# Kernel optimization log

Measured on AMD Instinct MI355X. Metric: run time of the kernel, lower is better.

## Reference

```python
import jax, jax.numpy as jnp
import numpy as np

N_NODES = 50000
N_EDGES = 800000
D_IN = 64
D_HID = 64
D_OUT = 64


def setup_inputs() -> dict:
    key = jax.random.key(0)
    ks = jax.random.split(key, 10)
    x = jax.random.normal(ks[0], (N_NODES, D_IN), dtype=jnp.float32)
    src = jax.random.randint(ks[1], (N_EDGES,), 0, N_NODES, dtype=jnp.int32)
    dst = jax.random.randint(ks[2], (N_EDGES,), 0, N_NODES, dtype=jnp.int32)
    s = 1.0 / np.sqrt(D_IN)
    W0 = jax.random.uniform(ks[3], (D_IN, D_HID), jnp.float32, -s, s)
    b0 = jnp.zeros((D_HID,), jnp.float32)
    W1 = jax.random.uniform(ks[4], (D_HID, D_HID), jnp.float32, -s, s)
    b1 = jnp.zeros((D_HID,), jnp.float32)
    W2 = jax.random.uniform(ks[5], (D_HID, D_OUT), jnp.float32, -s, s)
    b2 = jnp.zeros((D_OUT,), jnp.float32)
    return {"x": x, "src": src, "dst": dst, "W0": W0, "b0": b0,
            "W1": W1, "b1": b1, "W2": W2, "b2": b2}


def reference(x, src, dst, W0, b0, W1, b1, W2, b2):
    N = x.shape[0]
    # in-degree (constant across layers)
    deg = jax.ops.segment_sum(jnp.ones(src.shape[0], x.dtype), dst, num_segments=N)
    inv = (1.0 / (deg + 1.0))[:, None]  # [N,1] gcn normalizer (deg + self)

    def sage_gcn(h, W, b):
        # gather neighbor feats along edges, scatter-add to destinations
        agg = jax.ops.segment_sum(h[src], dst, num_segments=N)  # [N,d]
        h_neigh = (agg + h) * inv
        return h_neigh @ W + b

    h = sage_gcn(x, W0, b0)
    h = jax.nn.relu(h)
    h = sage_gcn(h, W1, b1)
    h = jax.nn.relu(h)
    h = sage_gcn(h, W2, b2)
    return h
```

## Files before the change

kernel.cpp:

```cpp
#include <hip/hip_runtime.h>

#define D 64

__global__ void count_deg_kernel(const int* __restrict__ dst, int* __restrict__ deg, int nE) {
    int e4 = (blockIdx.x * blockDim.x + threadIdx.x) * 4;
    if (e4 + 3 < nE) {
        int4 d = *(const int4*)(dst + e4);
        atomicAdd(&deg[d.x], 1);
        atomicAdd(&deg[d.y], 1);
        atomicAdd(&deg[d.z], 1);
        atomicAdd(&deg[d.w], 1);
    } else {
        for (int e = e4; e < nE; ++e) atomicAdd(&deg[dst[e]], 1);
    }
}

__global__ __launch_bounds__(256) void scan_a_kernel(const int* __restrict__ deg,
                                                     int* __restrict__ row_ptr,
                                                     int* __restrict__ blocksums, int N) {
    __shared__ int s[256];
    int t = threadIdx.x;
    int i = blockIdx.x * 256 + t;
    int v = (i < N) ? deg[i] : 0;
    s[t] = v;
    __syncthreads();
    #pragma unroll
    for (int d = 1; d < 256; d <<= 1) {
        int u = (t >= d) ? s[t - d] : 0;
        __syncthreads();
        s[t] += u;
        __syncthreads();
    }
    if (i < N) row_ptr[i] = s[t] - v;
    if (t == 255) blocksums[blockIdx.x] = s[255];
}

__global__ __launch_bounds__(256) void scan_b_kernel(int* __restrict__ blocksums,
                                                     int* __restrict__ row_ptr,
                                                     int nb, int N) {
    __shared__ int s[256];
    int t = threadIdx.x;
    int v = (t < nb) ? blocksums[t] : 0;
    s[t] = v;
    __syncthreads();
    #pragma unroll
    for (int d = 1; d < 256; d <<= 1) {
        int u = (t >= d) ? s[t - d] : 0;
        __syncthreads();
        s[t] += u;
        __syncthreads();
    }
    if (t < nb) blocksums[t] = s[t] - v;
    if (t == 255) row_ptr[N] = s[255];
}

__global__ __launch_bounds__(256) void scan_c_kernel(int* __restrict__ row_ptr,
                                                     int* __restrict__ cursor,
                                                     const int* __restrict__ blocksums, int N) {
    int i = blockIdx.x * 256 + threadIdx.x;
    if (i < N) {
        int r = row_ptr[i] + blocksums[blockIdx.x];
        row_ptr[i] = r;
        cursor[i] = r;
    }
}

__global__ __launch_bounds__(256) void fill_csr_sliced_kernel(
    const int* __restrict__ src, const int* __restrict__ dst,
    int* __restrict__ cursor, int* __restrict__ col,
    int nE, int slice_size)
{
    const int g  = blockIdx.x & 7;
    const int gb = blockIdx.x >> 3;
    const int lo = g * slice_size;
    const int hi = lo + slice_size;
    int e4 = (gb * 256 + (int)threadIdx.x) * 4;
    if (e4 + 3 < nE) {
        int4 d = *(const int4*)(dst + e4);
        bool m0 = (d.x >= lo) & (d.x < hi);
        bool m1 = (d.y >= lo) & (d.y < hi);
        bool m2 = (d.z >= lo) & (d.z < hi);
        bool m3 = (d.w >= lo) & (d.w < hi);
        if (m0 | m1 | m2 | m3) {
            int4 s = *(const int4*)(src + e4);
            if (m0) col[atomicAdd(&cursor[d.x], 1)] = s.x;
            if (m1) col[atomicAdd(&cursor[d.y], 1)] = s.y;
            if (m2) col[atomicAdd(&cursor[d.z], 1)] = s.z;
            if (m3) col[atomicAdd(&cursor[d.w], 1)] = s.w;
        }
    } else if (e4 < nE) {
        for (int e = e4; e < nE; ++e) {
            int dd = dst[e];
            if (dd >= lo && dd < hi) col[atomicAdd(&cursor[dd], 1)] = src[e];
        }
    }
}

__global__ __launch_bounds__(256, 4) void sage_layer_kernel(
    const float* __restrict__ h, const int* __restrict__ row_ptr,
    const int* __restrict__ col, const float* __restrict__ W,
    const float* __restrict__ bias, float* __restrict__ out,
    int N, int do_relu)
{
    const int lane = threadIdx.x & 63;
    const int sub  = lane >> 4;
    const int fq   = lane & 15;
    const int w    = threadIdx.x >> 6;

    float Wreg[D];
    #pragma unroll
    for (int k = 0; k < D; ++k) Wreg[k] = W[k * D + lane];
    const float bj = bias[lane];

    const float4* __restrict__ h4 = (const float4*)h;

    const int nwaves = gridDim.x * 4;
    for (int i0 = blockIdx.x * 4 + w; i0 < N; i0 += nwaves) {
        const int i   = __builtin_amdgcn_readfirstlane(i0);
        const int rs  = __builtin_amdgcn_readfirstlane(row_ptr[i]);
        const int re  = __builtin_amdgcn_readfirstlane(row_ptr[i + 1]);
        const int deg = re - rs;

        float4 a0 = {0,0,0,0}, a1 = {0,0,0,0}, a2 = {0,0,0,0}, a3 = {0,0,0,0};

        for (int e0 = rs; e0 < re; e0 += 64) {
            int ee = e0 + lane;
            int idxv = col[(ee < re) ? ee : (re - 1)];
            int rem = re - e0;
            int steps = (((rem < 64) ? rem : 64) + 3) >> 2;
            int t = 0;
            for (; t + 4 <= steps; t += 4) {
                int base = (t << 2) + sub;
                int s0 = __shfl(idxv, base);
                int s1 = __shfl(idxv, base + 4);
                int s2 = __shfl(idxv, base + 8);
                int s3 = __shfl(idxv, base + 12);
                float4 v0 = h4[(size_t)s0 * 16 + fq];
                float4 v1 = h4[(size_t)s1 * 16 + fq];
                float4 v2 = h4[(size_t)s2 * 16 + fq];
                float4 v3 = h4[(size_t)s3 * 16 + fq];
                a0.x += v0.x; a0.y += v0.y; a0.z += v0.z; a0.w += v0.w;
                a1.x += v1.x; a1.y += v1.y; a1.z += v1.z; a1.w += v1.w;
                a2.x += v2.x; a2.y += v2.y; a2.z += v2.z; a2.w += v2.w;
                a3.x += v3.x; a3.y += v3.y; a3.z += v3.z; a3.w += v3.w;
            }
            for (; t < steps; ++t) {
                int s0 = __shfl(idxv, (t << 2) + sub);
                float4 v0 = h4[(size_t)s0 * 16 + fq];
                a0.x += v0.x; a0.y += v0.y; a0.z += v0.z; a0.w += v0.w;
            }
        }

        float4 tt;
        tt.x = (a0.x + a1.x) + (a2.x + a3.x);
        tt.y = (a0.y + a1.y) + (a2.y + a3.y);
        tt.z = (a0.z + a1.z) + (a2.z + a3.z);
        tt.w = (a0.w + a1.w) + (a2.w + a3.w);
        tt.x += __shfl_xor(tt.x, 16); tt.x += __shfl_xor(tt.x, 32);
        tt.y += __shfl_xor(tt.y, 16); tt.y += __shfl_xor(tt.y, 32);
        tt.z += __shfl_xor(tt.z, 16); tt.z += __shfl_xor(tt.z, 32);
        tt.w += __shfl_xor(tt.w, 16); tt.w += __shfl_xor(tt.w, 32);

        int pad = (-deg) & 3;
        if (deg > 0 && pad) {
            int last = __builtin_amdgcn_readfirstlane(col[re - 1]);
            float4 vl = h4[(size_t)last * 16 + fq];
            float fp = (float)pad;
            tt.x = fmaf(-fp, vl.x, tt.x);
            tt.y = fmaf(-fp, vl.y, tt.y);
            tt.z = fmaf(-fp, vl.z, tt.z);
            tt.w = fmaf(-fp, vl.w, tt.w);
        }

        float4 hs = h4[(size_t)i * 16 + fq];
        float invd = 1.0f / (float)(deg + 1);
        tt.x = (tt.x + hs.x) * invd;
        tt.y = (tt.y + hs.y) * invd;
        tt.z = (tt.z + hs.z) * invd;
        tt.w = (tt.w + hs.w) * invd;

        float o = bj;
        #pragma unroll
        for (int k = 0; k < D; ++k) {
            float comp = ((k & 3) == 0) ? tt.x : ((k & 3) == 1) ? tt.y
                       : ((k & 3) == 2) ? tt.z : tt.w;
            int ti = __builtin_amdgcn_readlane(__float_as_int(comp), k >> 2);
            o = fmaf(__int_as_float(ti), Wreg[k], o);
        }
        if (do_relu) o = fmaxf(o, 0.0f);
        out[(size_t)i * D + lane] = o;
    }
}

extern "C" void kernel_launch(void* const* d_in, const int* in_sizes, int n_in,
                              void* d_out, int out_size, void* d_ws, size_t ws_size,
                              hipStream_t stream) {
    const float* x   = (const float*)d_in[0];
    const int*   src = (const int*)d_in[1];
    const int*   dst = (const int*)d_in[2];
    const float* W0  = (const float*)d_in[3];
    const float* b0  = (const float*)d_in[4];
    const float* W1  = (const float*)d_in[5];
    const float* b1  = (const float*)d_in[6];
    const float* W2  = (const float*)d_in[7];
    const float* b2  = (const float*)d_in[8];
    float* out = (float*)d_out;

    const int N = in_sizes[0] / D;
    const int E = in_sizes[1];

    const int scan_blocks = (N + 255) / 256;

    char* ws = (char*)d_ws;
    size_t off = 0;
    auto alloc = [&](size_t bytes) -> void* {
        void* p = ws + off;
        off = (off + bytes + 255) & ~(size_t)255;
        return p;
    };
    int*   deg       = (int*)  alloc((size_t)N * sizeof(int));
    int*   row_ptr   = (int*)  alloc((size_t)(N + 1) * sizeof(int));
    int*   cursor    = (int*)  alloc((size_t)N * sizeof(int));
    int*   blocksums = (int*)  alloc((size_t)scan_blocks * sizeof(int));
    int*   col       = (int*)  alloc((size_t)E * sizeof(int));
    float* h1        = (float*)alloc((size_t)N * D * sizeof(float));
    float* h2        = (float*)alloc((size_t)N * D * sizeof(float));

    hipMemsetAsync(deg, 0, (size_t)N * sizeof(int), stream);
    const int e4_blocks = (E / 4 + 255) / 256;
    count_deg_kernel<<<e4_blocks, 256, 0, stream>>>(dst, deg, E);
    scan_a_kernel<<<scan_blocks, 256, 0, stream>>>(deg, row_ptr, blocksums, N);
    scan_b_kernel<<<1, 256, 0, stream>>>(blocksums, row_ptr, scan_blocks, N);
    scan_c_kernel<<<scan_blocks, 256, 0, stream>>>(row_ptr, cursor, blocksums, N);
    const int slice_size = (N + 7) / 8;
    fill_csr_sliced_kernel<<<e4_blocks * 8, 256, 0, stream>>>(src, dst, cursor, col, E, slice_size);

    const int layer_blocks = 4096;

    sage_layer_kernel<<<layer_blocks, 256, 0, stream>>>(x,  row_ptr, col, W0, b0, h1,  N, 1);
    sage_layer_kernel<<<layer_blocks, 256, 0, stream>>>(h1, row_ptr, col, W1, b1, h2,  N, 1);
    sage_layer_kernel<<<layer_blocks, 256, 0, stream>>>(h2, row_ptr, col, W2, b2, out, N, 0);
}
```

Measured before the change: 289.0 us.

## Process two nodes per wave and slice degree counting by destination range

```diff
diff --git a/kernel.cpp b/kernel.cpp
--- a/kernel.cpp
+++ b/kernel.cpp
@@ -2,16 +2,24 @@
 
 #define D 64
 
-__global__ void count_deg_kernel(const int* __restrict__ dst, int* __restrict__ deg, int nE) {
-    int e4 = (blockIdx.x * blockDim.x + threadIdx.x) * 4;
+__global__ void count_deg_sliced_kernel(const int* __restrict__ dst, int* __restrict__ deg,
+                                        int nE, int slice_size) {
+    const int g  = blockIdx.x & 7;
+    const int gb = blockIdx.x >> 3;
+    const int lo = g * slice_size;
+    const int hi = lo + slice_size;
+    int e4 = (gb * 256 + (int)threadIdx.x) * 4;
     if (e4 + 3 < nE) {
         int4 d = *(const int4*)(dst + e4);
-        atomicAdd(&deg[d.x], 1);
-        atomicAdd(&deg[d.y], 1);
-        atomicAdd(&deg[d.z], 1);
-        atomicAdd(&deg[d.w], 1);
-    } else {
-        for (int e = e4; e < nE; ++e) atomicAdd(&deg[dst[e]], 1);
+        if (d.x >= lo && d.x < hi) atomicAdd(&deg[d.x], 1);
+        if (d.y >= lo && d.y < hi) atomicAdd(&deg[d.y], 1);
+        if (d.z >= lo && d.z < hi) atomicAdd(&deg[d.z], 1);
+        if (d.w >= lo && d.w < hi) atomicAdd(&deg[d.w], 1);
+    } else if (e4 < nE) {
+        for (int e = e4; e < nE; ++e) {
+            int dd = dst[e];
+            if (dd >= lo && dd < hi) atomicAdd(&deg[dd], 1);
+        }
     }
 }
 
@@ -106,89 +114,147 @@
     const int sub  = lane >> 4;
     const int fq   = lane & 15;
     const int w    = threadIdx.x >> 6;
-
-    float Wreg[D];
-    #pragma unroll
-    for (int k = 0; k < D; ++k) Wreg[k] = W[k * D + lane];
     const float bj = bias[lane];
 
     const float4* __restrict__ h4 = (const float4*)h;
-
     const int nwaves = gridDim.x * 4;
-    for (int i0 = blockIdx.x * 4 + w; i0 < N; i0 += nwaves) {
-        const int i   = __builtin_amdgcn_readfirstlane(i0);
-        const int rs  = __builtin_amdgcn_readfirstlane(row_ptr[i]);
-        const int re  = __builtin_amdgcn_readfirstlane(row_ptr[i + 1]);
-        const int deg = re - rs;
-
-        float4 a0 = {0,0,0,0}, a1 = {0,0,0,0}, a2 = {0,0,0,0}, a3 = {0,0,0,0};
-
-        for (int e0 = rs; e0 < re; e0 += 64) {
-            int ee = e0 + lane;
-            int idxv = col[(ee < re) ? ee : (re - 1)];
-            int rem = re - e0;
-            int steps = (((rem < 64) ? rem : 64) + 3) >> 2;
-            int t = 0;
-            for (; t + 4 <= steps; t += 4) {
-                int base = (t << 2) + sub;
-                int s0 = __shfl(idxv, base);
-                int s1 = __shfl(idxv, base + 4);
-                int s2 = __shfl(idxv, base + 8);
-                int s3 = __shfl(idxv, base + 12);
-                float4 v0 = h4[(size_t)s0 * 16 + fq];
-                float4 v1 = h4[(size_t)s1 * 16 + fq];
-                float4 v2 = h4[(size_t)s2 * 16 + fq];
-                float4 v3 = h4[(size_t)s3 * 16 + fq];
-                a0.x += v0.x; a0.y += v0.y; a0.z += v0.z; a0.w += v0.w;
-                a1.x += v1.x; a1.y += v1.y; a1.z += v1.z; a1.w += v1.w;
-                a2.x += v2.x; a2.y += v2.y; a2.z += v2.z; a2.w += v2.w;
-                a3.x += v3.x; a3.y += v3.y; a3.z += v3.z; a3.w += v3.w;
+
+    for (int p = (blockIdx.x * 4 + w) * 2; p < N; p += nwaves * 2) {
+        const int iA = __builtin_amdgcn_readfirstlane(p);
+        const int iB = iA + 1;
+        const bool hasB = (iB < N);
+
+        const int rsA = __builtin_amdgcn_readfirstlane(row_ptr[iA]);
+        const int reA = __builtin_amdgcn_readfirstlane(row_ptr[iA + 1]);
+        const int reB = hasB ? __builtin_amdgcn_readfirstlane(row_ptr[iB + 1]) : reA;
+        const int rsB = reA;
+        const int degA = reA - rsA;
+        const int degB = reB - rsB;
+
+        float4 aA0 = {0,0,0,0}, aA1 = {0,0,0,0}, aA2 = {0,0,0,0}, aA3 = {0,0,0,0};
+        float4 aB0 = {0,0,0,0}, aB1 = {0,0,0,0}, aB2 = {0,0,0,0}, aB3 = {0,0,0,0};
+
+        int eA = rsA, eB = rsB;
+        while ((eA < reA) | (eB < reB)) {
+            int idxA = 0, idxB = 0;
+            if (eA < reA) { int ee = eA + lane; idxA = col[(ee < reA) ? ee : (reA - 1)]; }
+            if (eB < reB) { int ee = eB + lane; idxB = col[(ee < reB) ? ee : (reB - 1)]; }
+
+            if (eA < reA) {
+                int rem = reA - eA;
+                int steps = (((rem < 64) ? rem : 64) + 3) >> 2;
+                int t = 0;
+                for (; t + 4 <= steps; t += 4) {
+                    int base = (t << 2) + sub;
+                    int s0 = __shfl(idxA, base);
+                    int s1 = __shfl(idxA, base + 4);
+                    int s2 = __shfl(idxA, base + 8);
+                    int s3 = __shfl(idxA, base + 12);
+                    float4 v0 = h4[(size_t)s0 * 16 + fq];
+                    float4 v1 = h4[(size_t)s1 * 16 + fq];
+                    float4 v2 = h4[(size_t)s2 * 16 + fq];
+                    float4 v3 = h4[(size_t)s3 * 16 + fq];
+                    aA0.x += v0.x; aA0.y += v0.y; aA0.z += v0.z; aA0.w += v0.w;
+                    aA1.x += v1.x; aA1.y += v1.y; aA1.z += v1.z; aA1.w += v1.w;
+                    aA2.x += v2.x; aA2.y += v2.y; aA2.z += v2.z; aA2.w += v2.w;
+                    aA3.x += v3.x; aA3.y += v3.y; aA3.z += v3.z; aA3.w += v3.w;
+                }
+                for (; t < steps; ++t) {
+                    int s0 = __shfl(idxA, (t << 2) + sub);
+                    float4 v0 = h4[(size_t)s0 * 16 + fq];
+                    aA0.x += v0.x; aA0.y += v0.y; aA0.z += v0.z; aA0.w += v0.w;
+                }
             }
-            for (; t < steps; ++t) {
-                int s0 = __shfl(idxv, (t << 2) + sub);
-                float4 v0 = h4[(size_t)s0 * 16 + fq];
-                a0.x += v0.x; a0.y += v0.y; a0.z += v0.z; a0.w += v0.w;
+            if (eB < reB) {
+                int rem = reB - eB;
+                int steps = (((rem < 64) ? rem : 64) + 3) >> 2;
+                int t = 0;
+                for (; t + 4 <= steps; t += 4) {
+                    int base = (t << 2) + sub;
+                    int s0 = __shfl(idxB, base);
+                    int s1 = __shfl(idxB, base + 4);
+                    int s2 = __shfl(idxB, base + 8);
+                    int s3 = __shfl(idxB, base + 12);
+                    float4 v0 = h4[(size_t)s0 * 16 + fq];
+                    float4 v1 = h4[(size_t)s1 * 16 + fq];
+                    float4 v2 = h4[(size_t)s2 * 16 + fq];
+                    float4 v3 = h4[(size_t)s3 * 16 + fq];
+                    aB0.x += v0.x; aB0.y += v0.y; aB0.z += v0.z; aB0.w += v0.w;
+                    aB1.x += v1.x; aB1.y += v1.y; aB1.z += v1.z; aB1.w += v1.w;
+                    aB2.x += v2.x; aB2.y += v2.y; aB2.z += v2.z; aB2.w += v2.w;
+                    aB3.x += v3.x; aB3.y += v3.y; aB3.z += v3.z; aB3.w += v3.w;
+                }
+                for (; t < steps; ++t) {
+                    int s0 = __shfl(idxB, (t << 2) + sub);
+                    float4 v0 = h4[(size_t)s0 * 16 + fq];
+                    aB0.x += v0.x; aB0.y += v0.y; aB0.z += v0.z; aB0.w += v0.w;
+                }
             }
-        }
-
-        float4 tt;
-        tt.x = (a0.x + a1.x) + (a2.x + a3.x);
-        tt.y = (a0.y + a1.y) + (a2.y + a3.y);
-        tt.z = (a0.z + a1.z) + (a2.z + a3.z);
-        tt.w = (a0.w + a1.w) + (a2.w + a3.w);
-        tt.x += __shfl_xor(tt.x, 16); tt.x += __shfl_xor(tt.x, 32);
-        tt.y += __shfl_xor(tt.y, 16); tt.y += __shfl_xor(tt.y, 32);
-        tt.z += __shfl_xor(tt.z, 16); tt.z += __shfl_xor(tt.z, 32);
-        tt.w += __shfl_xor(tt.w, 16); tt.w += __shfl_xor(tt.w, 32);
-
-        int pad = (-deg) & 3;
-        if (deg > 0 && pad) {
-            int last = __builtin_amdgcn_readfirstlane(col[re - 1]);
+            eA += 64; eB += 64;
+        }
+
+        float4 tA, tB;
+        tA.x = (aA0.x + aA1.x) + (aA2.x + aA3.x);
+        tA.y = (aA0.y + aA1.y) + (aA2.y + aA3.y);
+        tA.z = (aA0.z + aA1.z) + (aA2.z + aA3.z);
+        tA.w = (aA0.w + aA1.w) + (aA2.w + aA3.w);
+        tB.x = (aB0.x + aB1.x) + (aB2.x + aB3.x);
+        tB.y = (aB0.y + aB1.y) + (aB2.y + aB3.y);
+        tB.z = (aB0.z + aB1.z) + (aB2.z + aB3.z);
+        tB.w = (aB0.w + aB1.w) + (aB2.w + aB3.w);
+        tA.x += __shfl_xor(tA.x, 16); tA.x += __shfl_xor(tA.x, 32);
+        tA.y += __shfl_xor(tA.y, 16); tA.y += __shfl_xor(tA.y, 32);
+        tA.z += __shfl_xor(tA.z, 16); tA.z += __shfl_xor(tA.z, 32);
+        tA.w += __shfl_xor(tA.w, 16); tA.w += __shfl_xor(tA.w, 32);
+        tB.x += __shfl_xor(tB.x, 16); tB.x += __shfl_xor(tB.x, 32);
+        tB.y += __shfl_xor(tB.y, 16); tB.y += __shfl_xor(tB.y, 32);
+        tB.z += __shfl_xor(tB.z, 16); tB.z += __shfl_xor(tB.z, 32);
+        tB.w += __shfl_xor(tB.w, 16); tB.w += __shfl_xor(tB.w, 32);
+
+        int padA = (-degA) & 3;
+        if (degA > 0 && padA) {
+            int last = __builtin_amdgcn_readfirstlane(col[reA - 1]);
             float4 vl = h4[(size_t)last * 16 + fq];
-            float fp = (float)pad;
-            tt.x = fmaf(-fp, vl.x, tt.x);
-            tt.y = fmaf(-fp, vl.y, tt.y);
-            tt.z = fmaf(-fp, vl.z, tt.z);
-            tt.w = fmaf(-fp, vl.w, tt.w);
-        }
-
-        float4 hs = h4[(size_t)i * 16 + fq];
-        float invd = 1.0f / (float)(deg + 1);
-        tt.x = (tt.x + hs.x) * invd;
-        tt.y = (tt.y + hs.y) * invd;
-        tt.z = (tt.z + hs.z) * invd;
-        tt.w = (tt.w + hs.w) * invd;
-
-        float o = bj;
+            float fp = (float)padA;
+            tA.x = fmaf(-fp, vl.x, tA.x); tA.y = fmaf(-fp, vl.y, tA.y);
+            tA.z = fmaf(-fp, vl.z, tA.z); tA.w = fmaf(-fp, vl.w, tA.w);
+        }
+        int padB = (-degB) & 3;
+        if (hasB && degB > 0 && padB) {
+            int last = __builtin_amdgcn_readfirstlane(col[reB - 1]);
+            float4 vl = h4[(size_t)last * 16 + fq];
+            float fp = (float)padB;
+            tB.x = fmaf(-fp, vl.x, tB.x); tB.y = fmaf(-fp, vl.y, tB.y);
+            tB.z = fmaf(-fp, vl.z, tB.z); tB.w = fmaf(-fp, vl.w, tB.w);
+        }
+
+        float4 hsA = h4[(size_t)iA * 16 + fq];
+        float invA = 1.0f / (float)(degA + 1);
+        tA.x = (tA.x + hsA.x) * invA; tA.y = (tA.y + hsA.y) * invA;
+        tA.z = (tA.z + hsA.z) * invA; tA.w = (tA.w + hsA.w) * invA;
+        if (hasB) {
+            float4 hsB = h4[(size_t)iB * 16 + fq];
+            float invB = 1.0f / (float)(degB + 1);
+            tB.x = (tB.x + hsB.x) * invB; tB.y = (tB.y + hsB.y) * invB;
+            tB.z = (tB.z + hsB.z) * invB; tB.w = (tB.w + hsB.w) * invB;
+        }
+
+        float oA = bj, oB = bj;
         #pragma unroll
         for (int k = 0; k < D; ++k) {
-            float comp = ((k & 3) == 0) ? tt.x : ((k & 3) == 1) ? tt.y
-                       : ((k & 3) == 2) ? tt.z : tt.w;
-            int ti = __builtin_amdgcn_readlane(__float_as_int(comp), k >> 2);
-            o = fmaf(__int_as_float(ti), Wreg[k], o);
-        }
-        if (do_relu) o = fmaxf(o, 0.0f);
-        out[(size_t)i * D + lane] = o;
+            float wv = W[k * D + lane];
+            float cA = ((k & 3) == 0) ? tA.x : ((k & 3) == 1) ? tA.y
+                     : ((k & 3) == 2) ? tA.z : tA.w;
+            float cB = ((k & 3) == 0) ? tB.x : ((k & 3) == 1) ? tB.y
+                     : ((k & 3) == 2) ? tB.z : tB.w;
+            int ia = __builtin_amdgcn_readlane(__float_as_int(cA), k >> 2);
+            int ib = __builtin_amdgcn_readlane(__float_as_int(cB), k >> 2);
+            oA = fmaf(__int_as_float(ia), wv, oA);
+            oB = fmaf(__int_as_float(ib), wv, oB);
+        }
+        if (do_relu) { oA = fmaxf(oA, 0.0f); oB = fmaxf(oB, 0.0f); }
+        out[(size_t)iA * D + lane] = oA;
+        if (hasB) out[(size_t)iB * D + lane] = oB;
     }
 }
 
@@ -228,14 +294,14 @@
 
     hipMemsetAsync(deg, 0, (size_t)N * sizeof(int), stream);
     const int e4_blocks = (E / 4 + 255) / 256;
-    count_deg_kernel<<<e4_blocks, 256, 0, stream>>>(dst, deg, E);
+    const int slice_size = (N + 7) / 8;
+    count_deg_sliced_kernel<<<e4_blocks * 8, 256, 0, stream>>>(dst, deg, E, slice_size);
     scan_a_kernel<<<scan_blocks, 256, 0, stream>>>(deg, row_ptr, blocksums, N);
     scan_b_kernel<<<1, 256, 0, stream>>>(blocksums, row_ptr, scan_blocks, N);
     scan_c_kernel<<<scan_blocks, 256, 0, stream>>>(row_ptr, cursor, blocksums, N);
-    const int slice_size = (N + 7) / 8;
     fill_csr_sliced_kernel<<<e4_blocks * 8, 256, 0, stream>>>(src, dst, cursor, col, E, slice_size);
 
-    const int layer_blocks = 4096;
+    const int layer_blocks = (N / 2 + 3) / 4;
 
     sage_layer_kernel<<<layer_blocks, 256, 0, stream>>>(x,  row_ptr, col, W0, b0, h1,  N, 1);
     sage_layer_kernel<<<layer_blocks, 256, 0, stream>>>(h1, row_ptr, col, W1, b1, h2,  N, 1);
```

Result: slower. 309.6 us (+7.1%).

## Split SAGE layer into column-chunked gather and separate MLP kernels

Applied to the files above, without the earlier changes.

```diff
diff --git a/kernel.cpp b/kernel.cpp
--- a/kernel.cpp
+++ b/kernel.cpp
@@ -2,16 +2,24 @@
 
 #define D 64
 
-__global__ void count_deg_kernel(const int* __restrict__ dst, int* __restrict__ deg, int nE) {
-    int e4 = (blockIdx.x * blockDim.x + threadIdx.x) * 4;
+__global__ void count_deg_sliced_kernel(const int* __restrict__ dst, int* __restrict__ deg,
+                                        int nE, int slice_size) {
+    const int g  = blockIdx.x & 7;
+    const int gb = blockIdx.x >> 3;
+    const int lo = g * slice_size;
+    const int hi = lo + slice_size;
+    int e4 = (gb * 256 + (int)threadIdx.x) * 4;
     if (e4 + 3 < nE) {
         int4 d = *(const int4*)(dst + e4);
-        atomicAdd(&deg[d.x], 1);
-        atomicAdd(&deg[d.y], 1);
-        atomicAdd(&deg[d.z], 1);
-        atomicAdd(&deg[d.w], 1);
-    } else {
-        for (int e = e4; e < nE; ++e) atomicAdd(&deg[dst[e]], 1);
+        if (d.x >= lo && d.x < hi) atomicAdd(&deg[d.x], 1);
+        if (d.y >= lo && d.y < hi) atomicAdd(&deg[d.y], 1);
+        if (d.z >= lo && d.z < hi) atomicAdd(&deg[d.z], 1);
+        if (d.w >= lo && d.w < hi) atomicAdd(&deg[d.w], 1);
+    } else if (e4 < nE) {
+        for (int e = e4; e < nE; ++e) {
+            int dd = dst[e];
+            if (dd >= lo && dd < hi) atomicAdd(&deg[dd], 1);
+        }
     }
 }
 
@@ -96,96 +104,95 @@
     }
 }
 
-__global__ __launch_bounds__(256, 4) void sage_layer_kernel(
+__global__ __launch_bounds__(256, 4) void sage_gather_kernel(
     const float* __restrict__ h, const int* __restrict__ row_ptr,
-    const int* __restrict__ col, const float* __restrict__ W,
+    const int* __restrict__ col, float* __restrict__ t, int N)
+{
+    const int g     = blockIdx.x & 7;
+    const int chunk = g & 3;
+    const int half  = g >> 2;
+    const int gb    = blockIdx.x >> 3;
+    const int lane  = threadIdx.x & 63;
+    const int sub   = lane >> 4;
+    const int f     = lane & 15;
+    const int fcol  = chunk * 16 + f;
+    const int w     = threadIdx.x >> 6;
+
+    const int Nh = (N + 1) >> 1;
+    const int lo = half * Nh;
+    const int hi = (lo + Nh < N) ? (lo + Nh) : N;
+    const int waves_per_group = (gridDim.x >> 3) * 4;
+
+    for (int i0 = lo + gb * 4 + w; i0 < hi; i0 += waves_per_group) {
+        const int i  = __builtin_amdgcn_readfirstlane(i0);
+        const int rs = __builtin_amdgcn_readfirstlane(row_ptr[i]);
+        const int re = __builtin_amdgcn_readfirstlane(row_ptr[i + 1]);
+        const int deg = re - rs;
+
+        float a0 = 0.f, a1 = 0.f, a2 = 0.f, a3 = 0.f;
+        for (int e0 = rs; e0 < re; e0 += 64) {
+            int ee = e0 + lane;
+            int idx = col[(ee < re) ? ee : (re - 1)];
+            int rem = re - e0;
+            int steps = (((rem < 64) ? rem : 64) + 3) >> 2;
+            int tt = 0;
+            for (; tt + 4 <= steps; tt += 4) {
+                int base = (tt << 2) + sub;
+                int s0 = __shfl(idx, base);
+                int s1 = __shfl(idx, base + 4);
+                int s2 = __shfl(idx, base + 8);
+                int s3 = __shfl(idx, base + 12);
+                a0 += h[(size_t)s0 * D + fcol];
+                a1 += h[(size_t)s1 * D + fcol];
+                a2 += h[(size_t)s2 * D + fcol];
+                a3 += h[(size_t)s3 * D + fcol];
+            }
+            for (; tt < steps; ++tt) {
+                int s0 = __shfl(idx, (tt << 2) + sub);
+                a0 += h[(size_t)s0 * D + fcol];
+            }
+        }
+
+        float tv = (a0 + a1) + (a2 + a3);
+        tv += __shfl_xor(tv, 16);
+        tv += __shfl_xor(tv, 32);
+
+        int pad = (-deg) & 3;
+        if (deg > 0 && pad) {
+            int last = __builtin_amdgcn_readfirstlane(col[re - 1]);
+            tv = fmaf(-(float)pad, h[(size_t)last * D + fcol], tv);
+        }
+        tv = (tv + h[(size_t)i * D + fcol]) * (1.0f / (float)(deg + 1));
+
+        if (lane < 16) t[(size_t)i * D + fcol] = tv;
+    }
+}
+
+__global__ __launch_bounds__(256) void sage_mlp_kernel(
+    const float* __restrict__ t, const float* __restrict__ W,
     const float* __restrict__ bias, float* __restrict__ out,
     int N, int do_relu)
 {
+    __shared__ float Ws[D * D];
+    for (int i = threadIdx.x; i < D * D; i += 256) Ws[i] = W[i];
     const int lane = threadIdx.x & 63;
-    const int sub  = lane >> 4;
     const int fq   = lane & 15;
     const int w    = threadIdx.x >> 6;
-
-    float Wreg[D];
-    #pragma unroll
-    for (int k = 0; k < D; ++k) Wreg[k] = W[k * D + lane];
     const float bj = bias[lane];
-
-    const float4* __restrict__ h4 = (const float4*)h;
-
+    __syncthreads();
+
+    const float4* __restrict__ t4 = (const float4*)t;
     const int nwaves = gridDim.x * 4;
     for (int i0 = blockIdx.x * 4 + w; i0 < N; i0 += nwaves) {
-        const int i   = __builtin_amdgcn_readfirstlane(i0);
-        const int rs  = __builtin_amdgcn_readfirstlane(row_ptr[i]);
-        const int re  = __builtin_amdgcn_readfirstlane(row_ptr[i + 1]);
-        const int deg = re - rs;
-
-        float4 a0 = {0,0,0,0}, a1 = {0,0,0,0}, a2 = {0,0,0,0}, a3 = {0,0,0,0};
-
-        for (int e0 = rs; e0 < re; e0 += 64) {
-            int ee = e0 + lane;
-            int idxv = col[(ee < re) ? ee : (re - 1)];
-            int rem = re - e0;
-            int steps = (((rem < 64) ? rem : 64) + 3) >> 2;
-            int t = 0;
-            for (; t + 4 <= steps; t += 4) {
-                int base = (t << 2) + sub;
-                int s0 = __shfl(idxv, base);
-                int s1 = __shfl(idxv, base + 4);
-                int s2 = __shfl(idxv, base + 8);
-                int s3 = __shfl(idxv, base + 12);
-                float4 v0 = h4[(size_t)s0 * 16 + fq];
-                float4 v1 = h4[(size_t)s1 * 16 + fq];
-                float4 v2 = h4[(size_t)s2 * 16 + fq];
-                float4 v3 = h4[(size_t)s3 * 16 + fq];
-                a0.x += v0.x; a0.y += v0.y; a0.z += v0.z; a0.w += v0.w;
-                a1.x += v1.x; a1.y += v1.y; a1.z += v1.z; a1.w += v1.w;
-                a2.x += v2.x; a2.y += v2.y; a2.z += v2.z; a2.w += v2.w;
-                a3.x += v3.x; a3.y += v3.y; a3.z += v3.z; a3.w += v3.w;
-            }
-            for (; t < steps; ++t) {
-                int s0 = __shfl(idxv, (t << 2) + sub);
-                float4 v0 = h4[(size_t)s0 * 16 + fq];
-                a0.x += v0.x; a0.y += v0.y; a0.z += v0.z; a0.w += v0.w;
-            }
-        }
-
-        float4 tt;
-        tt.x = (a0.x + a1.x) + (a2.x + a3.x);
-        tt.y = (a0.y + a1.y) + (a2.y + a3.y);
-        tt.z = (a0.z + a1.z) + (a2.z + a3.z);
-        tt.w = (a0.w + a1.w) + (a2.w + a3.w);
-        tt.x += __shfl_xor(tt.x, 16); tt.x += __shfl_xor(tt.x, 32);
-        tt.y += __shfl_xor(tt.y, 16); tt.y += __shfl_xor(tt.y, 32);
-        tt.z += __shfl_xor(tt.z, 16); tt.z += __shfl_xor(tt.z, 32);
-        tt.w += __shfl_xor(tt.w, 16); tt.w += __shfl_xor(tt.w, 32);
-
-        int pad = (-deg) & 3;
-        if (deg > 0 && pad) {
-            int last = __builtin_amdgcn_readfirstlane(col[re - 1]);
-            float4 vl = h4[(size_t)last * 16 + fq];
-            float fp = (float)pad;
-            tt.x = fmaf(-fp, vl.x, tt.x);
-            tt.y = fmaf(-fp, vl.y, tt.y);
-            tt.z = fmaf(-fp, vl.z, tt.z);
-            tt.w = fmaf(-fp, vl.w, tt.w);
-        }
-
-        float4 hs = h4[(size_t)i * 16 + fq];
-        float invd = 1.0f / (float)(deg + 1);
-        tt.x = (tt.x + hs.x) * invd;
-        tt.y = (tt.y + hs.y) * invd;
-        tt.z = (tt.z + hs.z) * invd;
-        tt.w = (tt.w + hs.w) * invd;
-
+        const int i = __builtin_amdgcn_readfirstlane(i0);
+        float4 tv = t4[(size_t)i * 16 + fq];
         float o = bj;
         #pragma unroll
         for (int k = 0; k < D; ++k) {
-            float comp = ((k & 3) == 0) ? tt.x : ((k & 3) == 1) ? tt.y
-                       : ((k & 3) == 2) ? tt.z : tt.w;
+            float comp = ((k & 3) == 0) ? tv.x : ((k & 3) == 1) ? tv.y
+                       : ((k & 3) == 2) ? tv.z : tv.w;
             int ti = __builtin_amdgcn_readlane(__float_as_int(comp), k >> 2);
-            o = fmaf(__int_as_float(ti), Wreg[k], o);
+            o = fmaf(__int_as_float(ti), Ws[k * D + lane], o);
         }
         if (do_relu) o = fmaxf(o, 0.0f);
         out[(size_t)i * D + lane] = o;
@@ -225,19 +232,26 @@
     int*   col       = (int*)  alloc((size_t)E * sizeof(int));
     float* h1        = (float*)alloc((size_t)N * D * sizeof(float));
     float* h2        = (float*)alloc((size_t)N * D * sizeof(float));
+    float* t         = (float*)alloc((size_t)N * D * sizeof(float));
 
     hipMemsetAsync(deg, 0, (size_t)N * sizeof(int), stream);
     const int e4_blocks = (E / 4 + 255) / 256;
-    count_deg_kernel<<<e4_blocks, 256, 0, stream>>>(dst, deg, E);
+    const int slice_size = (N + 7) / 8;
+    count_deg_sliced_kernel<<<e4_blocks * 8, 256, 0, stream>>>(dst, deg, E, slice_size);
     scan_a_kernel<<<scan_blocks, 256, 0, stream>>>(deg, row_ptr, blocksums, N);
     scan_b_kernel<<<1, 256, 0, stream>>>(blocksums, row_ptr, scan_blocks, N);
     scan_c_kernel<<<scan_blocks, 256, 0, stream>>>(row_ptr, cursor, blocksums, N);
-    const int slice_size = (N + 7) / 8;
     fill_csr_sliced_kernel<<<e4_blocks * 8, 256, 0, stream>>>(src, dst, cursor, col, E, slice_size);
 
-    const int layer_blocks = 4096;
-
-    sage_layer_kernel<<<layer_blocks, 256, 0, stream>>>(x,  row_ptr, col, W0, b0, h1,  N, 1);
-    sage_layer_kernel<<<layer_blocks, 256, 0, stream>>>(h1, row_ptr, col, W1, b1, h2,  N, 1);
-    sage_layer_kernel<<<layer_blocks, 256, 0, stream>>>(h2, row_ptr, col, W2, b2, out, N, 0);
-}
+    const int gather_blocks = 2048;
+    const int mlp_blocks    = 2048;
+
+    sage_gather_kernel<<<gather_blocks, 256, 0, stream>>>(x, row_ptr, col, t, N);
+    sage_mlp_kernel<<<mlp_blocks, 256, 0, stream>>>(t, W0, b0, h1, N, 1);
+
+    sage_gather_kernel<<<gather_blocks, 256, 0, stream>>>(h1, row_ptr, col, t, N);
+    sage_mlp_kernel<<<mlp_blocks, 256, 0, stream>>>(t, W1, b1, h2, N, 1);
+
+    sage_gather_kernel<<<gather_blocks, 256, 0, stream>>>(h2, row_ptr, col, t, N);
+    sage_mlp_kernel<<<mlp_blocks, 256, 0, stream>>>(t, W2, b2, out, N, 0);
+}
```

Result: slower. 382.9 us (+32.5%).
